# Kernel optimization log

Hardware: AMD Instinct MI355X
Metric: run time of the kernel (lower is better)

Reference implementation:

```python
import jax, jax.numpy as jnp
from jax import lax
import numpy as np

FRAME_LEN = 128
HOP = 64  # frame_len // 2 (default hop)
SAMPLE_LEN = 65536
IR_LEN = 1024

# torch.hann_window(N) is periodic: 0.5*(1 - cos(2*pi*n/N))
WIN = 0.5 * (1.0 - jnp.cos(2.0 * jnp.pi * jnp.arange(FRAME_LEN, dtype=jnp.float32) / FRAME_LEN))


def setup_inputs() -> dict:
    key = jax.random.key(0)
    k1, k2 = jax.random.split(key)
    x = jax.random.normal(k1, (1, SAMPLE_LEN), dtype=jnp.float32)
    IR = jax.random.normal(k2, (1, IR_LEN), dtype=jnp.float32)
    return {"x": x, "IR": IR}


def _scale_ir(ir2d):
    # get_MSG + scale_IR(target_gain = MSG + 2)
    spec = jnp.fft.rfft(ir2d[0])
    mag = jnp.abs(spec)
    phase = jnp.angle(spec)
    power = mag ** 2
    MLG = jnp.mean(power)
    zero_phase = (phase > -0.1) & (phase < 0.1)  # DC bin always qualifies
    peak_gain = jnp.max(jnp.where(zero_phase, power, -jnp.inf))
    MSG = -10.0 * jnp.log10(peak_gain / MLG)
    target_gain = MSG + 2.0
    mean_gain = 10.0 * jnp.log10(MLG)
    factor = jnp.power(jnp.float32(0.5), (target_gain - mean_gain) / 6.0)
    return ir2d / factor


def _howling(x1d, ir1d):
    L = x1d.shape[0]
    conv_len = FRAME_LEN + ir1d.shape[0] - 1
    # number of iterations that perform the feedback update (torch loop breaks
    # when frame_start + conv_len >= sample_len, AFTER adding to howling_out)
    n_fb = max(0, (L - conv_len - 1) // HOP)

    def step(x, i):
        fs = i * HOP
        frame = lax.dynamic_slice(x, (fs,), (FRAME_LEN,))
        w = WIN * frame
        conv = jnp.convolve(w, ir1d)  # mode='full', length conv_len
        fs2 = fs + HOP
        seg = lax.dynamic_slice(x, (fs2,), (conv_len,)) + conv
        x = lax.dynamic_update_slice(x, seg, (fs2,))
        x = jnp.clip(x, -1.0, 1.0)
        return x, w

    x_out, frames = lax.scan(step, x1d, jnp.arange(n_fb))
    # last iteration: windowed frame added to howling_out, then break (no feedback, no clamp)
    fs_last = n_fb * HOP
    last_w = WIN * lax.dynamic_slice(x_out, (fs_last,), (FRAME_LEN,))
    frames = jnp.concatenate([frames, last_w[None, :]], axis=0)  # [T, frame_len]
    T = n_fb + 1
    pos = (jnp.arange(T)[:, None] * HOP + jnp.arange(FRAME_LEN)[None, :]).reshape(-1)
    howl = jnp.zeros((L,), x1d.dtype).at[pos].add(frames.reshape(-1))
    return jnp.clip(howl, -1.0, 1.0)


def reference(x, IR):
    ir = _scale_ir(IR)
    out = _howling(x[0], ir[0])
    return out[None, :]
```

## Files before the change

### kernel.cpp

```cpp
#include <hip/hip_runtime.h>
#include <math.h>

#define FRAME 128
#define HOPW 64
#define SLEN 65536
#define IRLEN 1024
#define NFB 1006
#define RMASK 2047
#define PI_D 3.14159265358979323846

__device__ __forceinline__ float clip1(float v) { return fminf(1.0f, fmaxf(-1.0f, v)); }

__device__ __forceinline__ void loop_barrier() {
    __builtin_amdgcn_sched_barrier(0);
    asm volatile("s_waitcnt lgkmcnt(0)" ::: "memory");
    __builtin_amdgcn_s_barrier();
    __builtin_amdgcn_sched_barrier(0);
}

__global__ __launch_bounds__(768) void howl_fused(const float* __restrict__ x,
                                                  const float* __restrict__ ir,
                                                  float* __restrict__ out) {
    __shared__ float ring[2048];
    __shared__ float part[2][4][1152];
    __shared__ float irl[IRLEN];
    __shared__ float wlds[FRAME];
    __shared__ float winv[FRAME];
    __shared__ float tailb[HOPW];
    __shared__ float red1[1024];
    __shared__ float red2[1024];
    __shared__ float invfs;

    const int tid = threadIdx.x;
    const int lane = tid & 63;
    const int kg = tid / 192;
    const int ob = tid % 192;
    const int q = ob * 6;
    const int lo = q - kg * 32 - 31;

    for (int idx = tid; idx < IRLEN; idx += 768) irl[idx] = ir[idx];
    for (int idx = tid; idx < 1216; idx += 768) ring[idx] = x[idx];
    if (tid < FRAME) winv[tid] = (float)(0.5 * (1.0 - cos(PI_D * (double)tid / 64.0)));
    if (tid < HOPW) tailb[tid] = 0.f;
    if (tid >= 513) { red1[tid] = -INFINITY; red2[tid] = 0.f; }
    if (tid < 256) { red1[768 + tid] = -INFINITY; red2[768 + tid] = 0.f; }
    __syncthreads();

    if (tid < 513) {
        double th = -2.0 * PI_D * (double)tid / 1024.0;
        double c4 = cos(4.0 * th), s4 = sin(4.0 * th);
        double wr0 = 1.0,           wi0 = 0.0;
        double wr1 = cos(th),       wi1 = sin(th);
        double wr2 = cos(2.0 * th), wi2 = sin(2.0 * th);
        double wr3 = cos(3.0 * th), wi3 = sin(3.0 * th);
        double ar0 = 0, ai0 = 0, ar1 = 0, ai1 = 0, ar2 = 0, ai2 = 0, ar3 = 0, ai3 = 0;
        for (int m = 0; m < 256; ++m) {
            double x0 = irl[4 * m], x1 = irl[4 * m + 1], x2 = irl[4 * m + 2], x3 = irl[4 * m + 3];
            ar0 += x0 * wr0; ai0 += x0 * wi0;
            ar1 += x1 * wr1; ai1 += x1 * wi1;
            ar2 += x2 * wr2; ai2 += x2 * wi2;
            ar3 += x3 * wr3; ai3 += x3 * wi3;
            double t;
            t = wr0 * c4 - wi0 * s4; wi0 = wr0 * s4 + wi0 * c4; wr0 = t;
            t = wr1 * c4 - wi1 * s4; wi1 = wr1 * s4 + wi1 * c4; wr1 = t;
            t = wr2 * c4 - wi2 * s4; wi2 = wr2 * s4 + wi2 * c4; wr2 = t;
            t = wr3 * c4 - wi3 * s4; wi3 = wr3 * s4 + wi3 * c4; wr3 = t;
        }
        double re = (ar0 + ar1) + (ar2 + ar3);
        double im = (ai0 + ai1) + (ai2 + ai3);
        float mag = (float)sqrt(re * re + im * im);
        float pw = mag * mag;
        double ph = atan2(im, re);
        int ok = (ph > -0.1 && ph < 0.1) ? 1 : 0;
        red1[tid] = ok ? pw : -INFINITY;
        red2[tid] = pw;
    }
    __syncthreads();
    for (int s = 512; s > 0; s >>= 1) {
        if (tid < s) {
            red1[tid] = fmaxf(red1[tid], red1[tid + s]);
            red2[tid] = red2[tid] + red2[tid + s];
        }
        __syncthreads();
    }
    if (tid == 0) {
        float peak = red1[0];
        float MLG = red2[0] / 513.0f;
        float MSG = -10.0f * log10f(peak / MLG);
        float target_gain = MSG + 2.0f;
        float mean_gain = 10.0f * log10f(MLG);
        invfs = powf(0.5f, (target_gain - mean_gain) / 6.0f);
    }
    __syncthreads();

    const float fbc = invfs;
    float wir[37];
#pragma unroll
    for (int j = 0; j < 37; ++j) {
        int idx = lo + j;
        wir[j] = (idx >= 0 && idx < IRLEN) ? irl[idx] / fbc : 0.f;
    }
    float xv = 0.f;
    if (tid >= 64 && tid < 128) xv = x[1216 + (tid - 64)];
    if (tid < FRAME) wlds[tid] = winv[tid] * ring[tid];
    __syncthreads();

    int pb = 0;
#pragma unroll 1
    for (int i = 0; i < NFB; ++i) {
        const int base = i * HOPW;

        float wreg = wlds[kg * 32 + (lane & 31)];

        if (tid < 64) {
            float w0 = wlds[tid];
            float w1 = wlds[64 + tid];
            out[base + tid] = clip1(w0 + tailb[tid]);
            tailb[tid] = w1;
        } else if (tid < 128) {
            int t = tid - 64;
            int pos = base + 1216 + t;
            if (pos < SLEN) ring[pos & RMASK] = clip1(xv);
            int npos = pos + HOPW;
            xv = (npos < SLEN) ? x[npos] : 0.f;
        }

        if (i > 0) {
            const float* pprev = &part[pb ^ 1][0][0];
            {
                int p = 128 + tid;
                int slot = (base + p) & RMASK;
                float s = pprev[p] + pprev[1152 + p] + pprev[2 * 1152 + p] + pprev[3 * 1152 + p];
                ring[slot] = clip1(ring[slot] + s);
            }
            if (tid >= 256 && tid < 512) {
                int p = 896 + (tid - 256);
                int slot = (base + p) & RMASK;
                float s = pprev[p] + pprev[1152 + p] + pprev[2 * 1152 + p] + pprev[3 * 1152 + p];
                ring[slot] = clip1(ring[slot] + s);
            }
        }

        float a0 = 0, a1 = 0, a2 = 0, a3 = 0, a4 = 0, a5 = 0;
#pragma unroll
        for (int kk = 0; kk < 32; ++kk) {
            float s = __int_as_float(__builtin_amdgcn_readlane(__float_as_int(wreg), 31 - kk));
            a0 = fmaf(s, wir[kk + 0], a0);
            a1 = fmaf(s, wir[kk + 1], a1);
            a2 = fmaf(s, wir[kk + 2], a2);
            a3 = fmaf(s, wir[kk + 3], a3);
            a4 = fmaf(s, wir[kk + 4], a4);
            a5 = fmaf(s, wir[kk + 5], a5);
        }
        float* pp = &part[pb][kg][q];
        *(float2*)(pp + 0) = make_float2(a0, a1);
        *(float2*)(pp + 2) = make_float2(a2, a3);
        *(float2*)(pp + 4) = make_float2(a4, a5);

        loop_barrier();

        if (tid < 128) {
            const float* pcur = &part[pb][0][0];
            int slot = (base + 64 + tid) & RMASK;
            float s = pcur[tid] + pcur[1152 + tid] + pcur[2 * 1152 + tid] + pcur[3 * 1152 + tid];
            float v = clip1(ring[slot] + s);
            ring[slot] = v;
            wlds[tid] = winv[tid] * v;
        }

        loop_barrier();
        pb ^= 1;
    }

    if (tid < 64) out[64384 + tid] = clip1(wlds[tid] + tailb[tid]);
    else if (tid < 128) out[64384 + tid] = clip1(wlds[tid]);
    for (int idx = 64512 + tid; idx < SLEN; idx += 768) out[idx] = 0.f;
}

extern "C" void kernel_launch(void* const* d_in, const int* in_sizes, int n_in,
                              void* d_out, int out_size, void* d_ws, size_t ws_size,
                              hipStream_t stream) {
    const float* x = (const float*)d_in[0];
    const float* ir = (const float*)d_in[1];
    float* out = (float*)d_out;
    (void)d_ws; (void)ws_size; (void)in_sizes; (void)n_in; (void)out_size;

    hipLaunchKernelGGL(howl_fused, dim3(1), dim3(768), 0, stream, x, ir, out);
}
```

Baseline: 1.058 ms.

## Keep windowed frame in registers per wave and defer ring writeback

Every wave now redundantly reduces the 128 fresh partial sums and computes the windowed frame in registers. This replaces the old path where 128 threads computed the frame and wrote it to LDS for all waves to read back. The ring update for those samples moves to the next iteration's accumulation pass, and the Hann window and overlap tail buffer become per-lane registers. The aim is to shorten the serial per-hop critical path by removing the LDS round trip and the imbalanced phase. The cost is extra redundant LDS reads and adds in every wave.

```diff
diff --git a/kernel.cpp b/kernel.cpp
--- a/kernel.cpp
+++ b/kernel.cpp
@@ -24,15 +24,13 @@
     __shared__ float ring[2048];
     __shared__ float part[2][4][1152];
     __shared__ float irl[IRLEN];
-    __shared__ float wlds[FRAME];
-    __shared__ float winv[FRAME];
-    __shared__ float tailb[HOPW];
     __shared__ float red1[1024];
     __shared__ float red2[1024];
     __shared__ float invfs;
 
     const int tid = threadIdx.x;
     const int lane = tid & 63;
+    const int wvid = tid >> 6;
     const int kg = tid / 192;
     const int ob = tid % 192;
     const int q = ob * 6;
@@ -40,8 +38,6 @@
 
     for (int idx = tid; idx < IRLEN; idx += 768) irl[idx] = ir[idx];
     for (int idx = tid; idx < 1216; idx += 768) ring[idx] = x[idx];
-    if (tid < FRAME) winv[tid] = (float)(0.5 * (1.0 - cos(PI_D * (double)tid / 64.0)));
-    if (tid < HOPW) tailb[tid] = 0.f;
     if (tid >= 513) { red1[tid] = -INFINITY; red2[tid] = 0.f; }
     if (tid < 256) { red1[768 + tid] = -INFINITY; red2[768 + tid] = 0.f; }
     __syncthreads();
@@ -100,9 +96,15 @@
         int idx = lo + j;
         wir[j] = (idx >= 0 && idx < IRLEN) ? irl[idx] / fbc : 0.f;
     }
+
+    const float hv0 = (float)(0.5 * (1.0 - cos(PI_D * (double)lane / 64.0)));
+    const float hv1 = (float)(0.5 * (1.0 - cos(PI_D * (double)(64 + lane) / 64.0)));
+    float w0 = hv0 * ring[lane];
+    float w1 = hv1 * ring[64 + lane];
+    float pw1 = 0.f;
     float xv = 0.f;
-    if (tid >= 64 && tid < 128) xv = x[1216 + (tid - 64)];
-    if (tid < FRAME) wlds[tid] = winv[tid] * ring[tid];
+    if (wvid == 1) xv = x[1216 + lane];
+    const int lbase = (kg & 1) * 32 + 31;
     __syncthreads();
 
     int pb = 0;
@@ -110,41 +112,36 @@
     for (int i = 0; i < NFB; ++i) {
         const int base = i * HOPW;
 
-        float wreg = wlds[kg * 32 + (lane & 31)];
-
-        if (tid < 64) {
-            float w0 = wlds[tid];
-            float w1 = wlds[64 + tid];
-            out[base + tid] = clip1(w0 + tailb[tid]);
-            tailb[tid] = w1;
-        } else if (tid < 128) {
-            int t = tid - 64;
-            int pos = base + 1216 + t;
+        if (wvid == 0) {
+            out[base + lane] = clip1(w0 + pw1);
+        } else if (wvid == 1) {
+            int pos = base + 1216 + lane;
             if (pos < SLEN) ring[pos & RMASK] = clip1(xv);
             int npos = pos + HOPW;
             xv = (npos < SLEN) ? x[npos] : 0.f;
         }
 
         if (i > 0) {
-            const float* pprev = &part[pb ^ 1][0][0];
+            const float* pp = &part[pb ^ 1][0][0];
             {
-                int p = 128 + tid;
+                int p = tid;
                 int slot = (base + p) & RMASK;
-                float s = pprev[p] + pprev[1152 + p] + pprev[2 * 1152 + p] + pprev[3 * 1152 + p];
+                float s = pp[p] + pp[1152 + p] + pp[2304 + p] + pp[3456 + p];
                 ring[slot] = clip1(ring[slot] + s);
             }
-            if (tid >= 256 && tid < 512) {
-                int p = 896 + (tid - 256);
+            if (tid >= 384) {
+                int p = 384 + tid;
                 int slot = (base + p) & RMASK;
-                float s = pprev[p] + pprev[1152 + p] + pprev[2 * 1152 + p] + pprev[3 * 1152 + p];
+                float s = pp[p] + pp[1152 + p] + pp[2304 + p] + pp[3456 + p];
                 ring[slot] = clip1(ring[slot] + s);
             }
         }
 
+        float wsrc = (kg < 2) ? w0 : w1;
         float a0 = 0, a1 = 0, a2 = 0, a3 = 0, a4 = 0, a5 = 0;
 #pragma unroll
         for (int kk = 0; kk < 32; ++kk) {
-            float s = __int_as_float(__builtin_amdgcn_readlane(__float_as_int(wreg), 31 - kk));
+            float s = __int_as_float(__builtin_amdgcn_readlane(__float_as_int(wsrc), lbase - kk));
             a0 = fmaf(s, wir[kk + 0], a0);
             a1 = fmaf(s, wir[kk + 1], a1);
             a2 = fmaf(s, wir[kk + 2], a2);
@@ -152,28 +149,33 @@
             a4 = fmaf(s, wir[kk + 4], a4);
             a5 = fmaf(s, wir[kk + 5], a5);
         }
-        float* pp = &part[pb][kg][q];
-        *(float2*)(pp + 0) = make_float2(a0, a1);
-        *(float2*)(pp + 2) = make_float2(a2, a3);
-        *(float2*)(pp + 4) = make_float2(a4, a5);
+        float* pw = &part[pb][kg][q];
+        *(float2*)(pw + 0) = make_float2(a0, a1);
+        *(float2*)(pw + 2) = make_float2(a2, a3);
+        *(float2*)(pw + 4) = make_float2(a4, a5);
 
         loop_barrier();
 
-        if (tid < 128) {
-            const float* pcur = &part[pb][0][0];
-            int slot = (base + 64 + tid) & RMASK;
-            float s = pcur[tid] + pcur[1152 + tid] + pcur[2 * 1152 + tid] + pcur[3 * 1152 + tid];
-            float v = clip1(ring[slot] + s);
-            ring[slot] = v;
-            wlds[tid] = winv[tid] * v;
+        {
+            const float* pc = &part[pb][0][0];
+            int c0 = lane, c1 = 64 + lane;
+            float s0 = pc[c0] + pc[1152 + c0] + pc[2304 + c0] + pc[3456 + c0];
+            float s1 = pc[c1] + pc[1152 + c1] + pc[2304 + c1] + pc[3456 + c1];
+            float v0 = clip1(ring[(base + 64 + c0) & RMASK] + s0);
+            float v1 = clip1(ring[(base + 64 + c1) & RMASK] + s1);
+            pw1 = w1;
+            w0 = hv0 * v0;
+            w1 = hv1 * v1;
         }
 
         loop_barrier();
         pb ^= 1;
     }
 
-    if (tid < 64) out[64384 + tid] = clip1(wlds[tid] + tailb[tid]);
-    else if (tid < 128) out[64384 + tid] = clip1(wlds[tid]);
+    if (wvid == 0) {
+        out[64384 + lane] = clip1(w0 + pw1);
+        out[64448 + lane] = clip1(w1);
+    }
     for (int idx = 64512 + tid; idx < SLEN; idx += 768) out[idx] = 0.f;
 }
 
```

Result: slower. 1.467 ms (+38.7%).

## Split convolution into critical head and deferred tail across warp roles

Applied to the files above, without the earlier changes.

Restructures the serial feedback loop so the convolution outputs needed by the next frame (the head, 128 samples) are computed first by a dedicated group of threads before the first barrier. The remaining tail outputs are computed after the barrier, concurrently with the ring/window update done by the first 128 threads. Previous-iteration partial sums are applied with float4 loads by a separate thread group, and the window values and tail buffer move from shared memory into registers. The aim is to shorten the per-iteration critical path between barriers. In exchange it adds register pressure and changes the order of clipping and summation.

```diff
diff --git a/kernel.cpp b/kernel.cpp
--- a/kernel.cpp
+++ b/kernel.cpp
@@ -21,27 +21,19 @@
 __global__ __launch_bounds__(768) void howl_fused(const float* __restrict__ x,
                                                   const float* __restrict__ ir,
                                                   float* __restrict__ out) {
-    __shared__ float ring[2048];
-    __shared__ float part[2][4][1152];
+    __shared__ __align__(16) float ring[2048];
+    __shared__ __align__(16) float part[2][4][1152];
     __shared__ float irl[IRLEN];
     __shared__ float wlds[FRAME];
-    __shared__ float winv[FRAME];
-    __shared__ float tailb[HOPW];
     __shared__ float red1[1024];
     __shared__ float red2[1024];
     __shared__ float invfs;
 
     const int tid = threadIdx.x;
     const int lane = tid & 63;
-    const int kg = tid / 192;
-    const int ob = tid % 192;
-    const int q = ob * 6;
-    const int lo = q - kg * 32 - 31;
 
     for (int idx = tid; idx < IRLEN; idx += 768) irl[idx] = ir[idx];
     for (int idx = tid; idx < 1216; idx += 768) ring[idx] = x[idx];
-    if (tid < FRAME) winv[tid] = (float)(0.5 * (1.0 - cos(PI_D * (double)tid / 64.0)));
-    if (tid < HOPW) tailb[tid] = 0.f;
     if (tid >= 513) { red1[tid] = -INFINITY; red2[tid] = 0.f; }
     if (tid < 256) { red1[768 + tid] = -INFINITY; red2[768 + tid] = 0.f; }
     __syncthreads();
@@ -76,10 +68,10 @@
         red2[tid] = pw;
     }
     __syncthreads();
-    for (int s = 512; s > 0; s >>= 1) {
-        if (tid < s) {
-            red1[tid] = fmaxf(red1[tid], red1[tid + s]);
-            red2[tid] = red2[tid] + red2[tid + s];
+    for (int st = 512; st > 0; st >>= 1) {
+        if (tid < st) {
+            red1[tid] = fmaxf(red1[tid], red1[tid + st]);
+            red2[tid] = red2[tid] + red2[tid + st];
         }
         __syncthreads();
     }
@@ -92,88 +84,130 @@
         invfs = powf(0.5f, (target_gain - mean_gain) / 6.0f);
     }
     __syncthreads();
-
     const float fbc = invfs;
-    float wir[37];
-#pragma unroll
-    for (int j = 0; j < 37; ++j) {
-        int idx = lo + j;
-        wir[j] = (idx >= 0 && idx < IRLEN) ? irl[idx] / fbc : 0.f;
-    }
-    float xv = 0.f;
-    if (tid >= 64 && tid < 128) xv = x[1216 + (tid - 64)];
-    if (tid < FRAME) wlds[tid] = winv[tid] * ring[tid];
-    __syncthreads();
-
-    int pb = 0;
+
+    float hvs = 0.f, tl = 0.f, xv = 0.f;
+    float wirH[32];
+    float wirT[39];
+    int kg32 = 0, pbase = 0, Ptail = 0;
+
+    if (tid < FRAME) {
+        hvs = (float)(0.5 * (1.0 - cos(PI_D * (double)tid / 64.0)));
+        wlds[tid] = hvs * ring[tid];
+        if (tid < HOPW) out[tid] = clip1(wlds[tid]);
+    }
+    if (tid >= 128 && tid < 640) {
+        int idx = tid - 128;
+        int kg = idx >> 7;
+        int obh = idx & 127;
+        kg32 = kg * 32;
+        pbase = kg * 1152;
+        Ptail = 128 + obh * 8;
+#pragma unroll
+        for (int j = 0; j < 32; ++j) {
+            int id = obh - kg32 - 31 + j;
+            wirH[j] = (id >= 0) ? irl[id] / fbc : 0.f;
+        }
+#pragma unroll
+        for (int m = 0; m < 39; ++m) {
+            int id = Ptail - kg32 - 31 + m;
+            wirT[m] = (id < IRLEN) ? irl[id] / fbc : 0.f;
+        }
+    }
+    if (tid >= 704) xv = x[1216 + (tid - 704)];
+    __syncthreads();
+
 #pragma unroll 1
     for (int i = 0; i < NFB; ++i) {
         const int base = i * HOPW;
-
-        float wreg = wlds[kg * 32 + (lane & 31)];
-
-        if (tid < 64) {
-            float w0 = wlds[tid];
-            float w1 = wlds[64 + tid];
-            out[base + tid] = clip1(w0 + tailb[tid]);
-            tailb[tid] = w1;
-        } else if (tid < 128) {
-            int t = tid - 64;
-            int pos = base + 1216 + t;
-            if (pos < SLEN) ring[pos & RMASK] = clip1(xv);
-            int npos = pos + HOPW;
-            xv = (npos < SLEN) ? x[npos] : 0.f;
-        }
-
-        if (i > 0) {
-            const float* pprev = &part[pb ^ 1][0][0];
-            {
-                int p = 128 + tid;
-                int slot = (base + p) & RMASK;
-                float s = pprev[p] + pprev[1152 + p] + pprev[2 * 1152 + p] + pprev[3 * 1152 + p];
-                ring[slot] = clip1(ring[slot] + s);
-            }
-            if (tid >= 256 && tid < 512) {
-                int p = 896 + (tid - 256);
-                int slot = (base + p) & RMASK;
-                float s = pprev[p] + pprev[1152 + p] + pprev[2 * 1152 + p] + pprev[3 * 1152 + p];
-                ring[slot] = clip1(ring[slot] + s);
-            }
-        }
-
-        float a0 = 0, a1 = 0, a2 = 0, a3 = 0, a4 = 0, a5 = 0;
-#pragma unroll
-        for (int kk = 0; kk < 32; ++kk) {
-            float s = __int_as_float(__builtin_amdgcn_readlane(__float_as_int(wreg), 31 - kk));
-            a0 = fmaf(s, wir[kk + 0], a0);
-            a1 = fmaf(s, wir[kk + 1], a1);
-            a2 = fmaf(s, wir[kk + 2], a2);
-            a3 = fmaf(s, wir[kk + 3], a3);
-            a4 = fmaf(s, wir[kk + 4], a4);
-            a5 = fmaf(s, wir[kk + 5], a5);
-        }
-        float* pp = &part[pb][kg][q];
-        *(float2*)(pp + 0) = make_float2(a0, a1);
-        *(float2*)(pp + 2) = make_float2(a2, a3);
-        *(float2*)(pp + 4) = make_float2(a4, a5);
-
+        float* cur = &part[i & 1][0][0];
+        float* prev = &part[(i + 1) & 1][0][0];
+
+        float ts[32];
+        if (tid >= 128 && tid < 640) {
+            float wreg = wlds[kg32 + (lane & 31)];
+#pragma unroll
+            for (int kk = 0; kk < 32; ++kk)
+                ts[kk] = __int_as_float(__builtin_amdgcn_readlane(__float_as_int(wreg), 31 - kk));
+            float ah = 0.f;
+#pragma unroll
+            for (int kk = 0; kk < 32; ++kk) ah = fmaf(ts[kk], wirH[kk], ah);
+            int obh = (tid - 128) & 127;
+            cur[pbase + obh] = ah;
+        } else if (tid < 64) {
+            tl = wlds[64 + lane];
+        }
         loop_barrier();
 
         if (tid < 128) {
-            const float* pcur = &part[pb][0][0];
-            int slot = (base + 64 + tid) & RMASK;
-            float s = pcur[tid] + pcur[1152 + tid] + pcur[2 * 1152 + tid] + pcur[3 * 1152 + tid];
-            float v = clip1(ring[slot] + s);
+            int s = tid;
+            int slot = (base + 64 + s) & RMASK;
+            float rr = ring[slot];
+            float sc4 = ((cur[s] + cur[1152 + s]) + cur[2304 + s]) + cur[3456 + s];
+            float v;
+            if (s >= 64 && i > 0) {
+                int t = 64 + s;
+                float pm = ((prev[t] + prev[1152 + t]) + prev[2304 + t]) + prev[3456 + t];
+                v = clip1(clip1(rr + pm) + sc4);
+            } else {
+                v = clip1(rr + sc4);
+            }
             ring[slot] = v;
-            wlds[tid] = winv[tid] * v;
-        }
-
+            float wn = hvs * v;
+            wlds[s] = wn;
+            if (s < 64) out[base + 64 + s] = clip1(wn + tl);
+        } else if (tid < 640) {
+            float a0 = 0, a1 = 0, a2 = 0, a3 = 0, a4 = 0, a5 = 0, a6 = 0, a7 = 0;
+#pragma unroll
+            for (int kk = 0; kk < 32; ++kk) {
+                float sc = ts[kk];
+                a0 = fmaf(sc, wirT[kk + 0], a0);
+                a1 = fmaf(sc, wirT[kk + 1], a1);
+                a2 = fmaf(sc, wirT[kk + 2], a2);
+                a3 = fmaf(sc, wirT[kk + 3], a3);
+                a4 = fmaf(sc, wirT[kk + 4], a4);
+                a5 = fmaf(sc, wirT[kk + 5], a5);
+                a6 = fmaf(sc, wirT[kk + 6], a6);
+                a7 = fmaf(sc, wirT[kk + 7], a7);
+            }
+            float* pw = cur + pbase + Ptail;
+            *(float4*)(pw + 0) = make_float4(a0, a1, a2, a3);
+            *(float4*)(pw + 4) = make_float4(a4, a5, a6, a7);
+        } else {
+            int a = tid - 640;
+            if (i > 0) {
+#pragma unroll
+                for (int r = 0; r < 2; ++r) {
+                    int q = a + r * 128;
+                    if (q < 240) {
+                        int p = 192 + 4 * q;
+                        float4 g0 = *(const float4*)&prev[p];
+                        float4 g1 = *(const float4*)&prev[1152 + p];
+                        float4 g2 = *(const float4*)&prev[2304 + p];
+                        float4 g3 = *(const float4*)&prev[3456 + p];
+                        int slot = (base + p) & RMASK;
+                        float4 rv = *(float4*)&ring[slot];
+                        rv.x = clip1(rv.x + (((g0.x + g1.x) + g2.x) + g3.x));
+                        rv.y = clip1(rv.y + (((g0.y + g1.y) + g2.y) + g3.y));
+                        rv.z = clip1(rv.z + (((g0.z + g1.z) + g2.z) + g3.z));
+                        rv.w = clip1(rv.w + (((g0.w + g1.w) + g2.w) + g3.w));
+                        *(float4*)&ring[slot] = rv;
+                    }
+                }
+            }
+            if (tid >= 704) {
+                int l = tid - 704;
+                int pos = base + 1216 + l;
+                if (pos < SLEN) ring[pos & RMASK] = clip1(xv);
+                int np = pos + HOPW;
+                xv = (np < SLEN) ? x[np] : 0.f;
+            }
+        }
         loop_barrier();
-        pb ^= 1;
-    }
-
-    if (tid < 64) out[64384 + tid] = clip1(wlds[tid] + tailb[tid]);
-    else if (tid < 128) out[64384 + tid] = clip1(wlds[tid]);
+    }
+
+    __syncthreads();
+    if (tid < 64) out[64448 + tid] = clip1(wlds[64 + tid]);
     for (int idx = 64512 + tid; idx < SLEN; idx += 768) out[idx] = 0.f;
 }
 
```

After: 2.966 ms. 2.8x slower.
